# Performance work log

Hardware: AMD Instinct MI355X
Metric: run time of the kernel (lower is better)

The kernel has to match this reference:

```python
import jax, jax.numpy as jnp
import numpy as np
from jax import lax

N_HARM = 64
N_BINS = 64
SR = 16000
B, T = 16, 64000


def setup_inputs() -> dict:
    key = jax.random.key(0)
    ks = jax.random.split(key, 12)
    audio = jax.random.normal(ks[0], (B, T), dtype=jnp.float32)
    # realistic fundamental frequencies in [80, 400) Hz
    f0 = 80.0 + 320.0 * jax.random.uniform(ks[1], (B, T), dtype=jnp.float32)
    white_noise = jax.random.normal(ks[2], (B, T), dtype=jnp.float32)
    def wconv(k, o, i, ksz):
        return jax.random.normal(k, (o, i, ksz), dtype=jnp.float32) * (1.0 / np.sqrt(i * ksz))
    w1 = wconv(ks[3], 32, 1, 9); b1 = jnp.zeros((32,), jnp.float32)
    w2 = wconv(ks[4], 64, 32, 9); b2 = jnp.zeros((64,), jnp.float32)
    w3 = wconv(ks[5], 128, 64, 9); b3 = jnp.zeros((128,), jnp.float32)
    wl = jax.random.normal(ks[6], (N_HARM + N_BINS, 128), dtype=jnp.float32) * (1.0 / np.sqrt(128))
    bl = jnp.zeros((N_HARM + N_BINS,), jnp.float32)
    return {"audio": audio, "f0": f0, "white_noise": white_noise,
            "w1": w1, "b1": b1, "w2": w2, "b2": b2, "w3": w3, "b3": b3,
            "wl": wl, "bl": bl}


def _conv1d(x, w, b):
    # x: [B, C_in, T], w: [C_out, C_in, K]; stride 2, pad 4
    y = lax.conv_general_dilated(x, w, window_strides=(2,), padding=[(4, 4)],
                                 dimension_numbers=("NCH", "OIH", "NCH"))
    return jax.nn.relu(y + b[None, :, None])


def reference(audio, f0, white_noise, w1, b1, w2, b2, w3, b3, wl, bl):
    batch, time = audio.shape
    # --- encoder ---
    x = audio[:, None, :]                    # [B, 1, T]
    x = _conv1d(x, w1, b1)                   # [B, 32, T/2]
    x = _conv1d(x, w2, b2)                   # [B, 64, T/4]
    x = _conv1d(x, w3, b3)                   # [B, 128, T/8]
    pooled = x.mean(axis=2)                  # AdaptiveAvgPool1d(1) + Flatten -> [B, 128]
    feats = pooled @ wl.T + bl               # [B, 128]
    # --- harmonic synth ---
    amps = jax.nn.relu(feats[:, :N_HARM])    # [B, H]; constant over time in original
    amps = amps / (amps.sum(axis=1, keepdims=True) + 1e-6)
    t = jnp.linspace(0.0, time / SR, time)   # endpoint-inclusive, as torch.linspace
    harm_idx = jnp.arange(1, N_HARM + 1, dtype=jnp.float32)
    # phase: [B, H, T] = 2*pi * (h * f0) * t
    phase = (2.0 * jnp.pi) * f0[:, None, :] * harm_idx[None, :, None] * t[None, None, :]
    harmonic_audio = jnp.einsum("bh,bht->bt", amps, jnp.sin(phase))
    # --- noise synth ---
    noise_mag = feats[:, N_HARM:]            # [B, n_bins]; mean over time of a constant = itself
    bin_size = time // N_BINS
    shaped = (white_noise.reshape(batch, N_BINS, bin_size) * noise_mag[:, :, None]).reshape(batch, time)
    return harmonic_audio + shaped
```

## Files before the change

kernel.cpp:

```cpp
#include <hip/hip_runtime.h>
#include <hip/hip_bf16.h>
#include <math.h>

typedef unsigned short u16;
typedef _Float16 f16x8 __attribute__((ext_vector_type(8)));
typedef float    f32x16 __attribute__((ext_vector_type(16)));
typedef u16      u16x8  __attribute__((ext_vector_type(8)));
typedef u16      u16x4  __attribute__((ext_vector_type(4)));

#define BATCH 16
#define T0 64000
#define T1 32000
#define T2 16000
#define T3 8000
#define NT3 250
#define NBLKX 32
#define NROWS1 1040

static __device__ __forceinline__ u16 f2h(float f) {
    _Float16 h = (_Float16)f;
    u16 u;
    __builtin_memcpy(&u, &h, 2);
    return u;
}

__global__ __launch_bounds__(256) void prep_w_k(const float* __restrict__ w2,
                                                const float* __restrict__ w3,
                                                u16* __restrict__ a2t,
                                                u16* __restrict__ a3t,
                                                float* __restrict__ pooled) {
    int idx = blockIdx.x * 256 + threadIdx.x;
    if (idx < 18432) {
        int j = idx & 7, o = (idx >> 3) & 63, g = (idx >> 9) & 3, kk = idx >> 11;
        a2t[idx] = f2h(w2[(o * 32 + g * 8 + j) * 9 + kk]);
    } else if (idx < 18432 + 73728) {
        int jdx = idx - 18432;
        int j = jdx & 7, o = (jdx >> 3) & 127, g = (jdx >> 10) & 7, kk = jdx >> 13;
        a3t[jdx] = f2h(w3[(o * 64 + g * 8 + j) * 9 + kk]);
    } else if (idx < 18432 + 73728 + 2048) {
        pooled[idx - 18432 - 73728] = 0.f;
    }
}

__global__ __launch_bounds__(512, 2) void mega_k(const float* __restrict__ audio,
                                                 const float* __restrict__ w1,
                                                 const float* __restrict__ b1,
                                                 const u16* __restrict__ a2t,
                                                 const float* __restrict__ b2,
                                                 const u16* __restrict__ a3t,
                                                 const float* __restrict__ b3,
                                                 float* __restrict__ pooled) {
    __shared__ u16 sm[520 * 64];
    const int tid = threadIdx.x;
    const int b = blockIdx.y;
    const int r0 = blockIdx.x * NT3;
    const int lane = tid & 63, wv = tid >> 6;
    const int ls = lane >> 5, ln = lane & 31;

    {
        const float* ar = audio + (size_t)b * T0;
        #pragma unroll
        for (int rep = 0; rep < 3; ++rep) {
            int l1 = rep * 512 + tid;
            if (l1 >= NROWS1) break;
            int t1 = 4 * r0 - 12 + l1;
            int rr = l1 >> 1, pp = l1 & 1;
            if (t1 < 0 || t1 >= T1) {
                u16x8 z;
                #pragma unroll
                for (int q = 0; q < 8; ++q) z[q] = 0;
                #pragma unroll
                for (int g = 0; g < 4; ++g) {
                    int slot = (pp * 4 + g) ^ (rr & 7);
                    *(u16x8*)(sm + rr * 64 + slot * 8) = z;
                }
            } else {
                int base = 2 * t1 - 4;
                float x[9];
                #pragma unroll
                for (int k = 0; k < 9; ++k) {
                    int t0v = base + k;
                    x[k] = (t0v >= 0 && t0v < T0) ? ar[t0v] : 0.f;
                }
                #pragma unroll
                for (int g = 0; g < 4; ++g) {
                    u16x8 v;
                    #pragma unroll
                    for (int j = 0; j < 8; ++j) {
                        int ch = g * 8 + j;
                        float acc = b1[ch];
                        #pragma unroll
                        for (int k = 0; k < 9; ++k) acc = fmaf(x[k], w1[ch * 9 + k], acc);
                        v[j] = f2h(fmaxf(acc, 0.f));
                    }
                    int slot = (pp * 4 + g) ^ (rr & 7);
                    *(u16x8*)(sm + rr * 64 + slot * 8) = v;
                }
            }
        }
    }
    __syncthreads();

    for (int cc = 0; cc < 2; ++cc) {
        int nl = cc * 256 + 32 * wv + ln;
        f32x16 acc2[2];
        #pragma unroll
        for (int mi = 0; mi < 2; ++mi)
            #pragma unroll
            for (int q = 0; q < 16; ++q) acc2[mi][q] = 0.f;
        f16x8 bfB[2];
        #pragma unroll 3
        for (int kk = 0; kk < 9; ++kk) {
            {
                int rr = nl + (kk >> 1);
                int pp = kk & 1;
                #pragma unroll
                for (int step = 0; step < 2; ++step) {
                    int slot = (pp * 4 + 2 * step + ls) ^ (rr & 7);
                    bfB[step] = *(const f16x8*)(sm + rr * 64 + slot * 8);
                }
            }
            const u16* ap = a2t + kk * 2048;
            #pragma unroll
            for (int step = 0; step < 2; ++step) {
                f16x8 af0 = *(const f16x8*)(ap + (2 * step + ls) * 512 + ln * 8);
                f16x8 af1 = *(const f16x8*)(ap + (2 * step + ls) * 512 + (32 + ln) * 8);
                acc2[0] = __builtin_amdgcn_mfma_f32_32x32x16_f16(af0, bfB[step], acc2[0], 0, 0, 0);
                acc2[1] = __builtin_amdgcn_mfma_f32_32x32x16_f16(af1, bfB[step], acc2[1], 0, 0, 0);
            }
        }
        __syncthreads();
        int l2 = nl;
        int t2 = 2 * r0 - 4 + l2;
        bool valid = (t2 >= 0) && (t2 < T2);
        #pragma unroll
        for (int mi = 0; mi < 2; ++mi)
            #pragma unroll
            for (int q = 0; q < 4; ++q) {
                u16x4 v;
                #pragma unroll
                for (int d = 0; d < 4; ++d) {
                    int o = 32 * mi + 8 * q + 4 * ls + d;
                    float xv = valid ? fmaxf(acc2[mi][4 * q + d] + b2[o], 0.f) : 0.f;
                    v[d] = f2h(xv);
                }
                int gy = 4 * mi + q;
                int sy = gy ^ ((l2 >> 1) & 7);
                *(u16x4*)(sm + l2 * 64 + sy * 8 + ls * 4) = v;
            }
        __syncthreads();
    }

    const int mh = wv & 1, nh = wv >> 1;
    f32x16 acc3[2][2];
    #pragma unroll
    for (int mi = 0; mi < 2; ++mi)
        #pragma unroll
        for (int ni = 0; ni < 2; ++ni)
            #pragma unroll
            for (int q = 0; q < 16; ++q) acc3[mi][ni][q] = 0.f;

    f16x8 bf[2][4];
    #pragma unroll 3
    for (int kk = 0; kk < 9; ++kk) {
        const u16* ap = a3t + kk * 8192;
        {
            #pragma unroll
            for (int ni = 0; ni < 2; ++ni) {
                int nl = 64 * nh + 32 * ni + ln;
                int l2 = 2 * nl + kk;
                int rrC = nl + (kk >> 1);
                #pragma unroll
                for (int step = 0; step < 4; ++step) {
                    int sy = (2 * step + ls) ^ (rrC & 7);
                    bf[ni][step] = *(const f16x8*)(sm + l2 * 64 + sy * 8);
                }
            }
        }
        #pragma unroll
        for (int step = 0; step < 4; ++step) {
            f16x8 af0 = *(const f16x8*)(ap + (2 * step + ls) * 1024 + (64 * mh + ln) * 8);
            f16x8 af1 = *(const f16x8*)(ap + (2 * step + ls) * 1024 + (64 * mh + 32 + ln) * 8);
            #pragma unroll
            for (int ni = 0; ni < 2; ++ni) {
                acc3[0][ni] = __builtin_amdgcn_mfma_f32_32x32x16_f16(af0, bf[ni][step], acc3[0][ni], 0, 0, 0);
                acc3[1][ni] = __builtin_amdgcn_mfma_f32_32x32x16_f16(af1, bf[ni][step], acc3[1][ni], 0, 0, 0);
            }
        }
    }

    float loc[32];
    #pragma unroll
    for (int mi = 0; mi < 2; ++mi)
        #pragma unroll
        for (int r = 0; r < 16; ++r) {
            int o = 64 * mh + 32 * mi + (r & 3) + 8 * (r >> 2) + 4 * ls;
            float bias = b3[o];
            float s = 0.f;
            #pragma unroll
            for (int ni = 0; ni < 2; ++ni) {
                int nl = 64 * nh + 32 * ni + ln;
                float v = fmaxf(acc3[mi][ni][r] + bias, 0.f);
                s += (nl < NT3) ? v : 0.f;
            }
            loc[mi * 16 + r] = s;
        }
    __syncthreads();
    float* smf = (float*)sm;
    #pragma unroll
    for (int mi = 0; mi < 2; ++mi)
        #pragma unroll
        for (int r = 0; r < 16; ++r) {
            int o = 64 * mh + 32 * mi + (r & 3) + 8 * (r >> 2) + 4 * ls;
            smf[nh * 4096 + o * 32 + ln] = loc[mi * 16 + r];
        }
    __syncthreads();
    if (tid < 128) {
        int o = tid;
        float s = 0.f;
        #pragma unroll
        for (int j = 0; j < 32; ++j) {
            int col = (j + o) & 31;
            s += smf[o * 32 + col] + smf[4096 + o * 32 + col]
               + smf[8192 + o * 32 + col] + smf[12288 + o * 32 + col];
        }
        atomicAdd(&pooled[b * 128 + o], s);
    }
}

__global__ __launch_bounds__(256) void synth_k(const float* __restrict__ f0,
                                               const float* __restrict__ wn,
                                               const float* __restrict__ pooled,
                                               const float* __restrict__ wl,
                                               const float* __restrict__ bl,
                                               float* __restrict__ out) {
    int tid = threadIdx.x;
    int b = blockIdx.y;
    __shared__ float pl[128];
    __shared__ float red[64];
    __shared__ float sa[64];
    __shared__ float nm[64];
    if (tid < 128) pl[tid] = pooled[b * 128 + tid] * (1.0f / 8000.0f);
    __syncthreads();
    float feat = 0.f;
    if (tid < 128) {
        feat = bl[tid];
        #pragma unroll 8
        for (int i = 0; i < 128; ++i) feat = fmaf(pl[i], wl[tid * 128 + i], feat);
    }
    if (tid < 64) red[tid] = fmaxf(feat, 0.f);
    __syncthreads();
    if (tid < 32) red[tid] += red[tid + 32];
    __syncthreads();
    if (tid < 16) red[tid] += red[tid + 16];
    __syncthreads();
    if (tid < 8) red[tid] += red[tid + 8];
    __syncthreads();
    if (tid < 4) red[tid] += red[tid + 4];
    __syncthreads();
    if (tid < 2) red[tid] += red[tid + 2];
    __syncthreads();
    if (tid == 0) red[0] += red[1];
    __syncthreads();
    float denom = red[0] + 1e-6f;
    if (tid < 64) sa[tid] = fmaxf(feat, 0.f) / denom;
    else if (tid < 128) nm[tid - 64] = feat;
    __syncthreads();
    int t = blockIdx.x * 256 + tid;
    float f0v = f0[(size_t)b * T0 + t];
    double u = (double)f0v * ((double)t * (4.0 / 63999.0));
    float uf = (float)(u - floor(u));
    float acc = 0.f;
    #pragma unroll
    for (int h = 1; h <= 64; ++h) {
        float x = uf * (float)h;
        x = x - floorf(x);
        acc = fmaf(sa[h - 1], __builtin_amdgcn_sinf(x), acc);
    }
    out[(size_t)b * T0 + t] = acc + wn[(size_t)b * T0 + t] * nm[t / 1000];
}

extern "C" void kernel_launch(void* const* d_in, const int* in_sizes, int n_in,
                              void* d_out, int out_size, void* d_ws, size_t ws_size,
                              hipStream_t stream) {
    const float* audio = (const float*)d_in[0];
    const float* f0    = (const float*)d_in[1];
    const float* wn    = (const float*)d_in[2];
    const float* w1    = (const float*)d_in[3];
    const float* b1    = (const float*)d_in[4];
    const float* w2    = (const float*)d_in[5];
    const float* b2    = (const float*)d_in[6];
    const float* w3    = (const float*)d_in[7];
    const float* b3    = (const float*)d_in[8];
    const float* wl    = (const float*)d_in[9];
    const float* bl    = (const float*)d_in[10];
    float* out = (float*)d_out;

    char* ws = (char*)d_ws;
    float* pooled = (float*)(ws);
    u16* a2t = (u16*)(ws + 8192);
    u16* a3t = (u16*)(ws + 8192 + 36864);

    prep_w_k<<<368, 256, 0, stream>>>(w2, w3, a2t, a3t, pooled);
    mega_k<<<dim3(NBLKX, BATCH), 512, 0, stream>>>(audio, w1, b1, a2t, b2, a3t, b3, pooled);
    synth_k<<<dim3(T0 / 256, BATCH), 256, 0, stream>>>(f0, wn, pooled, wl, bl, out);
}
```

Before: 156.3 us.

## Split feature head into own kernel and use Chebyshev recurrence for harmonics

Moves the linear head and amplitude normalisation into a small separate kernel, so each synth block no longer recomputes a 128x128 matvec and a multi-barrier reduction. The synth kernel now handles four samples per thread with float4 loads and stores. It replaces 64 hardware sin calls per sample with one sin/cos plus the Chebyshev recurrence sin((h+1)x) = 2cos(x)sin(hx) - sin((h-1)x). Error can accumulate over 64 harmonics in fp32, and the feature buffer reuses workspace that also holds the a2t weights, which mega_k has finished with by the time the head kernel runs.

```diff
diff --git a/kernel.cpp b/kernel.cpp
--- a/kernel.cpp
+++ b/kernel.cpp
@@ -228,56 +228,73 @@
     }
 }
 
+__global__ __launch_bounds__(128) void feats_k(const float* __restrict__ pooled,
+                                               const float* __restrict__ wl,
+                                               const float* __restrict__ bl,
+                                               float* __restrict__ featbuf) {
+    const int b = blockIdx.x;
+    const int tid = threadIdx.x;
+    __shared__ float pl[128];
+    pl[tid] = pooled[b * 128 + tid] * (1.0f / 8000.0f);
+    __syncthreads();
+    float feat = bl[tid];
+    #pragma unroll 8
+    for (int i = 0; i < 128; ++i) feat = fmaf(pl[i], wl[tid * 128 + i], feat);
+    if (tid < 64) {
+        float r = fmaxf(feat, 0.f);
+        float s = r;
+        #pragma unroll
+        for (int off = 32; off > 0; off >>= 1) s += __shfl_xor(s, off);
+        featbuf[b * 128 + tid] = r / (s + 1e-6f);
+    } else {
+        featbuf[b * 128 + tid] = feat;
+    }
+}
+
 __global__ __launch_bounds__(256) void synth_k(const float* __restrict__ f0,
                                                const float* __restrict__ wn,
-                                               const float* __restrict__ pooled,
-                                               const float* __restrict__ wl,
-                                               const float* __restrict__ bl,
+                                               const float* __restrict__ featbuf,
                                                float* __restrict__ out) {
-    int tid = threadIdx.x;
-    int b = blockIdx.y;
-    __shared__ float pl[128];
-    __shared__ float red[64];
+    const int tid = threadIdx.x;
+    const int b = blockIdx.y;
     __shared__ float sa[64];
     __shared__ float nm[64];
-    if (tid < 128) pl[tid] = pooled[b * 128 + tid] * (1.0f / 8000.0f);
-    __syncthreads();
-    float feat = 0.f;
-    if (tid < 128) {
-        feat = bl[tid];
-        #pragma unroll 8
-        for (int i = 0; i < 128; ++i) feat = fmaf(pl[i], wl[tid * 128 + i], feat);
-    }
-    if (tid < 64) red[tid] = fmaxf(feat, 0.f);
-    __syncthreads();
-    if (tid < 32) red[tid] += red[tid + 32];
-    __syncthreads();
-    if (tid < 16) red[tid] += red[tid + 16];
-    __syncthreads();
-    if (tid < 8) red[tid] += red[tid + 8];
-    __syncthreads();
-    if (tid < 4) red[tid] += red[tid + 4];
-    __syncthreads();
-    if (tid < 2) red[tid] += red[tid + 2];
-    __syncthreads();
-    if (tid == 0) red[0] += red[1];
-    __syncthreads();
-    float denom = red[0] + 1e-6f;
-    if (tid < 64) sa[tid] = fmaxf(feat, 0.f) / denom;
-    else if (tid < 128) nm[tid - 64] = feat;
-    __syncthreads();
-    int t = blockIdx.x * 256 + tid;
-    float f0v = f0[(size_t)b * T0 + t];
-    double u = (double)f0v * ((double)t * (4.0 / 63999.0));
-    float uf = (float)(u - floor(u));
-    float acc = 0.f;
-    #pragma unroll
-    for (int h = 1; h <= 64; ++h) {
-        float x = uf * (float)h;
-        x = x - floorf(x);
-        acc = fmaf(sa[h - 1], __builtin_amdgcn_sinf(x), acc);
-    }
-    out[(size_t)b * T0 + t] = acc + wn[(size_t)b * T0 + t] * nm[t / 1000];
+    if (tid < 64) sa[tid] = featbuf[b * 128 + tid];
+    else if (tid < 128) nm[tid - 64] = featbuf[b * 128 + tid];
+    __syncthreads();
+
+    const int t0v = blockIdx.x * 1024 + tid * 4;
+    if (t0v >= T0) return;
+
+    const float4 fv = *(const float4*)(f0 + (size_t)b * T0 + t0v);
+    const float4 wv = *(const float4*)(wn + (size_t)b * T0 + t0v);
+
+    float sc[4], sp[4], tc[4], ac[4];
+    #pragma unroll
+    for (int s = 0; s < 4; ++s) {
+        double u = (double)((&fv.x)[s]) * ((double)(t0v + s) * (4.0 / 63999.0));
+        float uf = (float)(u - floor(u));
+        sc[s] = __builtin_amdgcn_sinf(uf);
+        tc[s] = 2.0f * __builtin_amdgcn_cosf(uf);
+        sp[s] = 0.f;
+        ac[s] = 0.f;
+    }
+    #pragma unroll
+    for (int h = 0; h < 64; ++h) {
+        float a = sa[h];
+        #pragma unroll
+        for (int s = 0; s < 4; ++s) {
+            ac[s] = fmaf(a, sc[s], ac[s]);
+            float sn = fmaf(tc[s], sc[s], -sp[s]);
+            sp[s] = sc[s];
+            sc[s] = sn;
+        }
+    }
+    float4 o;
+    #pragma unroll
+    for (int s = 0; s < 4; ++s)
+        (&o.x)[s] = ac[s] + (&wv.x)[s] * nm[(t0v + s) / 1000];
+    *(float4*)(out + (size_t)b * T0 + t0v) = o;
 }
 
 extern "C" void kernel_launch(void* const* d_in, const int* in_sizes, int n_in,
@@ -300,8 +317,10 @@
     float* pooled = (float*)(ws);
     u16* a2t = (u16*)(ws + 8192);
     u16* a3t = (u16*)(ws + 8192 + 36864);
+    float* featbuf = (float*)(ws + 8192);
 
     prep_w_k<<<368, 256, 0, stream>>>(w2, w3, a2t, a3t, pooled);
     mega_k<<<dim3(NBLKX, BATCH), 512, 0, stream>>>(audio, w1, b1, a2t, b2, a3t, b3, pooled);
-    synth_k<<<dim3(T0 / 256, BATCH), 256, 0, stream>>>(f0, wn, pooled, wl, bl, out);
-}
+    feats_k<<<16, 128, 0, stream>>>(pooled, wl, bl, featbuf);
+    synth_k<<<dim3((T0 + 1023) / 1024, BATCH), 256, 0, stream>>>(f0, wn, featbuf, out);
+}
```

New measurement: 130.9 us. 16.2% less time.
